# Performance work log

Hardware: AMD Instinct MI355X
Metric: run time of the kernel (lower is better)

The kernel has to match this reference:

```python
import jax, jax.numpy as jnp
import numpy as np

EMB = 1024
HEADS = 16
HEAD_DIM = EMB // HEADS
SCALE = 1.0 / np.sqrt(HEAD_DIM)


def setup_inputs() -> dict:
    key = jax.random.key(0)
    ks = jax.random.split(key, 11)
    B, L, E = 4, 2048, EMB
    s = 1.0 / np.sqrt(E)
    inp = {
        "Q": jax.random.normal(ks[0], (B, L, E), jnp.float32),
        "K": jax.random.normal(ks[1], (B, L, E), jnp.float32),
        "V": jax.random.normal(ks[2], (B, L, E), jnp.float32),
        "WQ": jax.random.normal(ks[3], (E, E), jnp.float32) * s,
        "bQ": jax.random.normal(ks[4], (E,), jnp.float32) * s,
        "WK": jax.random.normal(ks[5], (E, E), jnp.float32) * s,
        "bK": jax.random.normal(ks[6], (E,), jnp.float32) * s,
        "WV": jax.random.normal(ks[7], (E, E), jnp.float32) * s,
        "bV": jax.random.normal(ks[8], (E,), jnp.float32) * s,
        "WO": jax.random.normal(ks[9], (E, E), jnp.float32) * s,
        "bO": jax.random.normal(ks[10], (E,), jnp.float32) * s,
    }
    return inp


def reference(Q, K, V, WQ, bQ, WK, bK, WV, bV, WO, bO):
    B, L, E = Q.shape
    # linear projections (torch Linear stores W as [out,in]; here W is [in,out])
    q = Q @ WQ + bQ
    k = K @ WK + bK
    v = V @ WV + bV
    # split heads: [B, H, L, D]
    q = q.reshape(B, L, HEADS, HEAD_DIM).transpose(0, 2, 1, 3)
    k = k.reshape(B, L, HEADS, HEAD_DIM).transpose(0, 2, 1, 3)
    v = v.reshape(B, L, HEADS, HEAD_DIM).transpose(0, 2, 1, 3)
    scores = jnp.einsum("bhqd,bhkd->bhqk", q, k) * SCALE
    # causal mask (mask=True): -inf above diagonal
    causal = jnp.tril(jnp.ones((L, L), dtype=bool))
    scores = jnp.where(causal, scores, -jnp.inf)
    probs = jax.nn.softmax(scores, axis=-1)
    out = jnp.einsum("bhqk,bhkd->bhqd", probs, v)  # [B,H,L,D]
    out = out.transpose(0, 2, 1, 3).reshape(B, L, E)  # concat heads
    return out @ WO + bO
```

## Files before the change

kernel.cpp:

```cpp
#include <hip/hip_runtime.h>
#include <hip/hip_bf16.h>

#define BB 4
#define HH 16
#define LL 2048
#define DD 64
#define EE 1024
#define MM (BB*LL)
#define SCL 0.125f
#define L2E 1.44269504f

using bf16   = __hip_bfloat16;
using bf16x8 = __attribute__((ext_vector_type(8))) __bf16;
using s16x4  = __attribute__((ext_vector_type(4))) short;
using f32x4  = __attribute__((ext_vector_type(4))) float;
using u32x4  = __attribute__((ext_vector_type(4))) unsigned int;
typedef unsigned int u32;

__device__ __forceinline__ bf16x8 ld8(const bf16* p){ return *(const bf16x8*)p; }
__device__ __forceinline__ bf16x8 ld8(const float* p){
  u32x4 a = *(const u32x4*)p;
  u32x4 b = *(const u32x4*)(p + 4);
  union { bf16x8 v; unsigned short s[8]; } r;
#pragma unroll
  for (int i = 0; i < 4; i++) r.s[i]     = (unsigned short)((a[i] + 0x7FFFu + ((a[i] >> 16) & 1u)) >> 16);
#pragma unroll
  for (int i = 0; i < 4; i++) r.s[i + 4] = (unsigned short)((b[i] + 0x7FFFu + ((b[i] >> 16) & 1u)) >> 16);
  return r.v;
}
__device__ __forceinline__ float ldf(const bf16* p){ return __bfloat162float(*p); }
__device__ __forceinline__ float ldf(const float* p){ return *p; }
__device__ __forceinline__ bf16 to_b(bf16 v){ return v; }
__device__ __forceinline__ bf16 to_b(float v){ return __float2bfloat16(v); }

__device__ __forceinline__ void async16(const bf16* g, bf16* l) {
  __builtin_amdgcn_global_load_lds((const __attribute__((address_space(1))) u32*)g,
                                   (__attribute__((address_space(3))) u32*)l, 16, 0, 0);
}

__global__ __launch_bounds__(256) void detect_dtype(const unsigned int* __restrict__ w,
                                                    int* __restrict__ flag) {
  __shared__ int cnt[256];
  int tid = threadIdx.x;
  int c = 0;
  for (int i = 0; i < 16; i++) {
    unsigned u = w[tid * 16 + i];
    unsigned e = (u >> 7) & 0xFF;
    c += (e >= 100 && e <= 140) ? 1 : 0;
  }
  cnt[tid] = c;
  __syncthreads();
  for (int s = 128; s > 0; s >>= 1) {
    if (tid < s) cnt[tid] += cnt[tid + s];
    __syncthreads();
  }
  if (tid == 0) *flag = (cnt[0] > 2048) ? 1 : 0;
}

__global__ __launch_bounds__(256) void convert_in(
    const void* __restrict__ X0, const void* __restrict__ X1, const void* __restrict__ X2,
    bf16* __restrict__ Y0, bf16* __restrict__ Y1, bf16* __restrict__ Y2,
    const int* __restrict__ flag) {
  int z = blockIdx.z;
  const void* X = (z == 0) ? X0 : (z == 1) ? X1 : X2;
  bf16* Y       = (z == 0) ? Y0 : (z == 1) ? Y1 : Y2;
  size_t idx = ((size_t)blockIdx.x * 256 + threadIdx.x) * 8;
  if (*flag) *(bf16x8*)(Y + idx) = *(const bf16x8*)((const bf16*)X + idx);
  else       *(bf16x8*)(Y + idx) = ld8((const float*)X + idx);
}

template<typename T>
__device__ __forceinline__ void tr_body(const T* __restrict__ W, bf16* __restrict__ Wt,
                                        bf16 (*t)[33]) {
  int tx = threadIdx.x, ty = threadIdx.y;
  int x = blockIdx.x * 32 + tx;
  for (int r = 0; r < 4; r++)
    t[ty + r * 8][tx] = to_b(W[(blockIdx.y * 32 + ty + r * 8) * EE + x]);
  __syncthreads();
  int x2 = blockIdx.y * 32 + tx;
  for (int r = 0; r < 4; r++)
    Wt[(blockIdx.x * 32 + ty + r * 8) * EE + x2] = t[tx][ty + r * 8];
}

__global__ __launch_bounds__(256) void transpose_w4(
    const void* __restrict__ W0, const void* __restrict__ W1,
    const void* __restrict__ W2, const void* __restrict__ W3,
    bf16* __restrict__ T0, bf16* __restrict__ T1,
    bf16* __restrict__ T2, bf16* __restrict__ T3,
    const int* __restrict__ flag) {
  __shared__ bf16 t[32][33];
  int z = blockIdx.z;
  const void* W = (z == 0) ? W0 : (z == 1) ? W1 : (z == 2) ? W2 : W3;
  bf16* Wt      = (z == 0) ? T0 : (z == 1) ? T1 : (z == 2) ? T2 : T3;
  if (*flag) tr_body<bf16>((const bf16*)W, Wt, t);
  else       tr_body<float>((const float*)W, Wt, t);
}

template<typename TIO>
__device__ void gemm_body(const bf16* __restrict__ A, const bf16* __restrict__ Bt,
                          const TIO* __restrict__ bias, void* __restrict__ Cv,
                          int mode, bf16* As, bf16* Bs) {
  constexpr int K = EE;
  int tid = threadIdx.x;
  int lane = tid & 63, w = tid >> 6;
  int l16 = lane & 15, quad = lane >> 4;
  int linear = blockIdx.x + 8 * blockIdx.y;
  int xcd = linear & 7;
  int slot = linear >> 3;
  int m0 = (xcd * 8 + (slot & 7)) * 128;
  int n0 = (slot >> 3) * 128;
  int mw = (w & 1) * 64;
  int nw = (w >> 1) * 64;
  int lr = lane >> 2;
  int lc = (lane & 3) * 8;

  f32x4 acc[4][4] = {};

  for (int k0 = 0; k0 < K; k0 += 32) {
    __syncthreads();
#pragma unroll
    for (int s = 0; s < 2; s++) {
      int r = w * 32 + s * 16;
      async16(A  + (size_t)(m0 + r + lr) * K + k0 + lc, As + r * 32);
      async16(Bt + (size_t)(n0 + r + lr) * K + k0 + lc, Bs + r * 32);
    }
    __syncthreads();
    bf16x8 af[4], bfr[4];
#pragma unroll
    for (int t = 0; t < 4; t++) {
      af[t]  = *(const bf16x8*)(As + (mw + t * 16 + l16) * 32 + quad * 8);
      bfr[t] = *(const bf16x8*)(Bs + (nw + t * 16 + l16) * 32 + quad * 8);
    }
#pragma unroll
    for (int mt = 0; mt < 4; mt++)
#pragma unroll
      for (int nt = 0; nt < 4; nt++)
        acc[mt][nt] = __builtin_amdgcn_mfma_f32_16x16x32_bf16(af[mt], bfr[nt], acc[mt][nt], 0, 0, 0);
  }

#pragma unroll
  for (int nt = 0; nt < 4; nt++) {
    int col = n0 + nw + nt * 16 + l16;
    float bv = ldf(bias + col);
    int hh = col >> 6, d = col & 63;
#pragma unroll
    for (int mt = 0; mt < 4; mt++) {
      f32x4 v = acc[mt][nt];
      int rowb = m0 + mw + mt * 16 + quad * 4;
      if (mode == 0) {
#pragma unroll
        for (int i = 0; i < 4; i++)
          ((bf16*)Cv)[(size_t)(rowb + i) * EE + col] = __float2bfloat16(v[i] + bv);
      } else if (mode == 3) {
#pragma unroll
        for (int i = 0; i < 4; i++) {
          float val = v[i] + bv;
          if constexpr (__is_same(TIO, bf16))
            ((bf16*)Cv)[(size_t)(rowb + i) * EE + col] = __float2bfloat16(val);
          else
            ((float*)Cv)[(size_t)(rowb + i) * EE + col] = val;
        }
      } else {
        int b = rowb >> 11, l0 = rowb & 2047;
        union { s16x4 p; bf16 e[4]; } u;
#pragma unroll
        for (int i = 0; i < 4; i++) u.e[i] = __float2bfloat16(v[i] + bv);
        *(s16x4*)((bf16*)Cv + ((size_t)(b * HH + hh) * DD + d) * LL + l0) = u.p;
      }
    }
  }
}

__global__ __launch_bounds__(256) void qkv_gemm(
    const bf16* __restrict__ Qc, const bf16* __restrict__ Kc, const bf16* __restrict__ Vc,
    const bf16* __restrict__ WQt, const bf16* __restrict__ WKt, const bf16* __restrict__ WVt,
    const void* __restrict__ bQ, const void* __restrict__ bK, const void* __restrict__ bV,
    bf16* __restrict__ qo, bf16* __restrict__ ko, bf16* __restrict__ vo,
    const int* __restrict__ flag) {
  __shared__ __align__(16) bf16 As[128 * 32];
  __shared__ __align__(16) bf16 Bs[128 * 32];
  int z = blockIdx.z;
  const bf16* A    = (z == 0) ? Qc  : (z == 1) ? Kc  : Vc;
  const bf16* Bt   = (z == 0) ? WQt : (z == 1) ? WKt : WVt;
  const void* bb   = (z == 0) ? bQ  : (z == 1) ? bK  : bV;
  bf16* C          = (z == 0) ? qo  : (z == 1) ? ko  : vo;
  int mode = (z == 2) ? 2 : 0;
  if (*flag) gemm_body<bf16>(A, Bt, (const bf16*)bb, C, mode, As, Bs);
  else       gemm_body<float>(A, Bt, (const float*)bb, C, mode, As, Bs);
}

__global__ __launch_bounds__(256) void out_gemm(const bf16* __restrict__ A,
                                                const bf16* __restrict__ WOt,
                                                const void* __restrict__ bO,
                                                void* __restrict__ C,
                                                const int* __restrict__ flag) {
  __shared__ __align__(16) bf16 As[128 * 32];
  __shared__ __align__(16) bf16 Bs[128 * 32];
  if (*flag) gemm_body<bf16>(A, WOt, (const bf16*)bO, C, 3, As, Bs);
  else       gemm_body<float>(A, WOt, (const float*)bO, C, 3, As, Bs);
}

__global__ __launch_bounds__(256) void attn(const bf16* __restrict__ qg,
                                            const bf16* __restrict__ kg,
                                            const bf16* __restrict__ vg,
                                            bf16* __restrict__ outg) {
  __shared__ __align__(16) bf16 Ks[2][64 * 64];
  __shared__ __align__(16) bf16 Vs[2][64 * 64];
  int linear = blockIdx.x + 16 * blockIdx.y;
  int xcd = linear & 7;
  int slot = linear >> 3;
  int bh = xcd * 8 + (slot & 7);
  int pb = slot >> 3;
  int tid = threadIdx.x;
  int w = tid >> 6, lane = tid & 63, l16 = lane & 15, quad = lane >> 4;
  int b = bh >> 4, hh = bh & 15;

  const bf16* qp = qg + (size_t)b * LL * EE + hh * DD;
  const bf16* kp = kg + (size_t)b * LL * EE + hh * DD;
  const bf16* vp = vg + (size_t)bh * DD * LL;
  const f32x4 z4 = {};
  int x7 = l16 & 7;

  for (int half = 0; half < 2; half++) {
    int tile = half ? (31 - pb) : pb;
    int qrow0 = tile * 64 + w * 16;
    int q = qrow0 + l16;
    bf16x8 bq0 = *(const bf16x8*)(qp + (size_t)q * EE + quad * 8);
    bf16x8 bq1 = *(const bf16x8*)(qp + (size_t)q * EE + 32 + quad * 8);

    float m = -1.0e30f, l = 0.f;
    f32x4 o[4] = {};
    int kend = tile + 1;

    __syncthreads();
    {
      int kbase = 0;
#pragma unroll
      for (int t = 0; t < 2; t++) {
        int R = w * 16 + t * 8;
        int r = R + (lane >> 3);
        int gb = (lane & 7) ^ (r & 7);
        async16(kp + (size_t)(kbase + r) * EE + gb * 8, &Ks[0][R * 64]);
        async16(vp + (size_t)r * LL + kbase + gb * 8, &Vs[0][R * 64]);
      }
    }

    for (int kb = 0; kb < kend; kb++) {
      int kbase = kb * 64;
      __syncthreads();
      if (kb + 1 < kend) {
        int nb = (kb + 1) & 1;
        int nbase = kbase + 64;
#pragma unroll
        for (int t = 0; t < 2; t++) {
          int R = w * 16 + t * 8;
          int r = R + (lane >> 3);
          int gb = (lane & 7) ^ (r & 7);
          async16(kp + (size_t)(nbase + r) * EE + gb * 8, &Ks[nb][R * 64]);
          async16(vp + (size_t)r * LL + nbase + gb * 8, &Vs[nb][R * 64]);
        }
      }
      const bf16* Kb = &Ks[kb & 1][0];
      const bf16* Vb = &Vs[kb & 1][0];

      f32x4 s[4];
#pragma unroll
      for (int kt = 0; kt < 4; kt++) {
        int row = kt * 16 + l16;
        bf16x8 kf0 = *(const bf16x8*)(Kb + row * 64 + (quad ^ x7) * 8);
        bf16x8 kf1 = *(const bf16x8*)(Kb + row * 64 + ((quad + 4) ^ x7) * 8);
        s[kt] = __builtin_amdgcn_mfma_f32_16x16x32_bf16(kf0, bq0, z4, 0, 0, 0);
        s[kt] = __builtin_amdgcn_mfma_f32_16x16x32_bf16(kf1, bq1, s[kt], 0, 0, 0);
      }
#if __has_builtin(__builtin_amdgcn_mfma_f32_16x16x16bf16_1k)
      s16x4 vf[4][4];
#pragma unroll
      for (int j = 0; j < 4; j++)
#pragma unroll
        for (int kt = 0; kt < 4; kt++)
          vf[j][kt] = *(const s16x4*)(Vb + (j * 16 + l16) * 64 +
                                      ((kt * 2 + (quad >> 1)) ^ x7) * 8 + (quad & 1) * 4);
#endif
      float sv[16];
      if (kbase + 63 <= qrow0) {
#pragma unroll
        for (int kt = 0; kt < 4; kt++)
#pragma unroll
          for (int i = 0; i < 4; i++) sv[kt * 4 + i] = s[kt][i] * SCL;
      } else {
        int rel = q - kbase - quad * 4;
#pragma unroll
        for (int kt = 0; kt < 4; kt++)
#pragma unroll
          for (int i = 0; i < 4; i++)
            sv[kt * 4 + i] = (kt * 16 + i <= rel) ? s[kt][i] * SCL : -1.0e30f;
      }
      float mloc = sv[0];
#pragma unroll
      for (int i = 1; i < 16; i++) mloc = fmaxf(mloc, sv[i]);
      mloc = fmaxf(mloc, __shfl_xor(mloc, 16));
      mloc = fmaxf(mloc, __shfl_xor(mloc, 32));
      float mnew = fmaxf(m, mloc);
      float alpha = exp2f((m - mnew) * L2E);
      float p[16], ssum = 0.f;
#pragma unroll
      for (int i = 0; i < 16; i++) { p[i] = exp2f((sv[i] - mnew) * L2E); ssum += p[i]; }
      ssum += __shfl_xor(ssum, 16);
      ssum += __shfl_xor(ssum, 32);
      l = l * alpha + ssum;
      m = mnew;
#pragma unroll
      for (int j = 0; j < 4; j++)
#pragma unroll
        for (int i = 0; i < 4; i++) o[j][i] *= alpha;
      union { s16x4 v4; bf16 e[4]; unsigned u[2]; } pk[4];
#pragma unroll
      for (int kt = 0; kt < 4; kt++)
#pragma unroll
        for (int i = 0; i < 4; i++) pk[kt].e[i] = __float2bfloat16(p[kt * 4 + i]);
#if __has_builtin(__builtin_amdgcn_mfma_f32_16x16x16bf16_1k)
#pragma unroll
      for (int kt = 0; kt < 4; kt++)
#pragma unroll
        for (int j = 0; j < 4; j++)
          o[j] = __builtin_amdgcn_mfma_f32_16x16x16bf16_1k(vf[j][kt], pk[kt].v4, o[j], 0, 0, 0);
#else
#pragma unroll
      for (int c = 0; c < 2; c++) {
        union { bf16x8 v8; unsigned u[4]; } bfr;
#pragma unroll
        for (int r = 0; r < 4; r++) {
          int key = c * 32 + quad * 8 + 2 * r;
          int srcl = (((key >> 2) & 3) << 4) + l16;
          unsigned v0 = __shfl((int)pk[2 * c].u[r & 1], srcl, 64);
          unsigned v1 = __shfl((int)pk[2 * c + 1].u[r & 1], srcl, 64);
          bfr.u[r] = (quad < 2) ? v0 : v1;
        }
#pragma unroll
        for (int j = 0; j < 4; j++) {
          bf16x8 vfr = *(const bf16x8*)(Vb + (j * 16 + l16) * 64 + ((c * 4 + quad) ^ x7) * 8);
          o[j] = __builtin_amdgcn_mfma_f32_16x16x32_bf16(vfr, bfr.v8, o[j], 0, 0, 0);
        }
      }
#endif
    }
    float inv = 1.0f / l;
#pragma unroll
    for (int j = 0; j < 4; j++) {
      union { s16x4 v4; bf16 e[4]; } u;
#pragma unroll
      for (int i = 0; i < 4; i++) u.e[i] = __float2bfloat16(o[j][i] * inv);
      *(s16x4*)(outg + (size_t)(b * LL + q) * EE + hh * DD + j * 16 + quad * 4) = u.v4;
    }
  }
}

extern "C" void kernel_launch(void* const* d_in, const int* in_sizes, int n_in,
                              void* d_out, int out_size, void* d_ws, size_t ws_size,
                              hipStream_t stream) {
  const void* Q   = d_in[0];
  const void* Kin = d_in[1];
  const void* V   = d_in[2];
  const void* WQ  = d_in[3];
  const void* bQ  = d_in[4];
  const void* WK  = d_in[5];
  const void* bK  = d_in[6];
  const void* WV  = d_in[7];
  const void* bV  = d_in[8];
  const void* WO  = d_in[9];
  const void* bO  = d_in[10];

  int* flag = (int*)d_ws;
  bf16* base = (bf16*)((char*)d_ws + 256);
  bf16* wqt  = base;
  bf16* wkt  = wqt + (size_t)EE * EE;
  bf16* wvt  = wkt + (size_t)EE * EE;
  bf16* wot  = wvt + (size_t)EE * EE;
  bf16* Qc   = wot + (size_t)EE * EE;
  bf16* Kc   = Qc  + (size_t)MM * EE;
  bf16* Vc   = Kc  + (size_t)MM * EE;
  bf16* qws  = Vc  + (size_t)MM * EE;
  bf16* kws  = qws + (size_t)MM * EE;
  bf16* vws  = kws + (size_t)MM * EE;
  bf16* aout = vws + (size_t)MM * EE;

  detect_dtype<<<1, 256, 0, stream>>>((const unsigned int*)WQ, flag);

  convert_in<<<dim3(MM * EE / 8 / 256, 1, 3), 256, 0, stream>>>(Q, Kin, V, Qc, Kc, Vc, flag);

  transpose_w4<<<dim3(32, 32, 4), dim3(32, 8), 0, stream>>>(
      WQ, WK, WV, WO, wqt, wkt, wvt, wot, flag);

  qkv_gemm<<<dim3(8, 64, 3), 256, 0, stream>>>(
      Qc, Kc, Vc, wqt, wkt, wvt, bQ, bK, bV, qws, kws, vws, flag);

  attn<<<dim3(16, 64), 256, 0, stream>>>(qws, kws, vws, aout);

  out_gemm<<<dim3(8, 64), 256, 0, stream>>>(aout, wot, bO, d_out, flag);
}
```

Measured before the change: 436.2 us.

## Fuse input conversion into QKV GEMM, widen K tile, enlarge attention query tiles

Drops the separate fp32-to-bf16 conversion pass: the QKV GEMM now reads the fp32 activations directly and converts them into shared memory, which saves a full write and re-read of three large tensors. The GEMM K-step doubles to 64, halving the number of barrier pairs per output tile at the cost of twice the shared memory. Attention now gives each wave 32 query rows (two 16-row groups) so every K/V tile is reused across more queries, uses a simpler grid mapping, and skips compute on fully masked key blocks. The fp32 A path uses synchronous loads instead of async copies, which may expose latency, and the larger per-wave state raises register pressure.

```diff
diff --git a/kernel.cpp b/kernel.cpp
--- a/kernel.cpp
+++ b/kernel.cpp
@@ -57,18 +57,6 @@
   if (tid == 0) *flag = (cnt[0] > 2048) ? 1 : 0;
 }
 
-__global__ __launch_bounds__(256) void convert_in(
-    const void* __restrict__ X0, const void* __restrict__ X1, const void* __restrict__ X2,
-    bf16* __restrict__ Y0, bf16* __restrict__ Y1, bf16* __restrict__ Y2,
-    const int* __restrict__ flag) {
-  int z = blockIdx.z;
-  const void* X = (z == 0) ? X0 : (z == 1) ? X1 : X2;
-  bf16* Y       = (z == 0) ? Y0 : (z == 1) ? Y1 : Y2;
-  size_t idx = ((size_t)blockIdx.x * 256 + threadIdx.x) * 8;
-  if (*flag) *(bf16x8*)(Y + idx) = *(const bf16x8*)((const bf16*)X + idx);
-  else       *(bf16x8*)(Y + idx) = ld8((const float*)X + idx);
-}
-
 template<typename T>
 __device__ __forceinline__ void tr_body(const T* __restrict__ W, bf16* __restrict__ Wt,
                                         bf16 (*t)[33]) {
@@ -96,8 +84,8 @@
   else       tr_body<float>((const float*)W, Wt, t);
 }
 
-template<typename TIO>
-__device__ void gemm_body(const bf16* __restrict__ A, const bf16* __restrict__ Bt,
+template<typename TA, typename TIO>
+__device__ void gemm_body(const TA* __restrict__ A, const bf16* __restrict__ Bt,
                           const TIO* __restrict__ bias, void* __restrict__ Cv,
                           int mode, bf16* As, bf16* Bs) {
   constexpr int K = EE;
@@ -111,31 +99,39 @@
   int n0 = (slot >> 3) * 128;
   int mw = (w & 1) * 64;
   int nw = (w >> 1) * 64;
-  int lr = lane >> 2;
-  int lc = (lane & 3) * 8;
+  int lr = lane >> 3;
+  int lc = (lane & 7) * 8;
 
   f32x4 acc[4][4] = {};
 
-  for (int k0 = 0; k0 < K; k0 += 32) {
+  for (int k0 = 0; k0 < K; k0 += 64) {
     __syncthreads();
 #pragma unroll
-    for (int s = 0; s < 2; s++) {
-      int r = w * 32 + s * 16;
-      async16(A  + (size_t)(m0 + r + lr) * K + k0 + lc, As + r * 32);
-      async16(Bt + (size_t)(n0 + r + lr) * K + k0 + lc, Bs + r * 32);
+    for (int t = 0; t < 4; t++) {
+      int R = w * 32 + t * 8;
+      int r = R + lr;
+      if constexpr (__is_same(TA, bf16)) {
+        async16(A + (size_t)(m0 + r) * K + k0 + lc, As + R * 64);
+      } else {
+        *(bf16x8*)(As + r * 64 + lc) = ld8(A + (size_t)(m0 + r) * K + k0 + lc);
+      }
+      async16(Bt + (size_t)(n0 + r) * K + k0 + lc, Bs + R * 64);
     }
     __syncthreads();
-    bf16x8 af[4], bfr[4];
-#pragma unroll
-    for (int t = 0; t < 4; t++) {
-      af[t]  = *(const bf16x8*)(As + (mw + t * 16 + l16) * 32 + quad * 8);
-      bfr[t] = *(const bf16x8*)(Bs + (nw + t * 16 + l16) * 32 + quad * 8);
-    }
-#pragma unroll
-    for (int mt = 0; mt < 4; mt++)
-#pragma unroll
-      for (int nt = 0; nt < 4; nt++)
-        acc[mt][nt] = __builtin_amdgcn_mfma_f32_16x16x32_bf16(af[mt], bfr[nt], acc[mt][nt], 0, 0, 0);
+#pragma unroll
+    for (int h = 0; h < 2; h++) {
+      bf16x8 af[4], bfr[4];
+#pragma unroll
+      for (int t = 0; t < 4; t++) {
+        af[t]  = *(const bf16x8*)(As + (mw + t * 16 + l16) * 64 + h * 32 + quad * 8);
+        bfr[t] = *(const bf16x8*)(Bs + (nw + t * 16 + l16) * 64 + h * 32 + quad * 8);
+      }
+#pragma unroll
+      for (int mt = 0; mt < 4; mt++)
+#pragma unroll
+        for (int nt = 0; nt < 4; nt++)
+          acc[mt][nt] = __builtin_amdgcn_mfma_f32_16x16x32_bf16(af[mt], bfr[nt], acc[mt][nt], 0, 0, 0);
+    }
   }
 
 #pragma unroll
@@ -172,21 +168,21 @@
 }
 
 __global__ __launch_bounds__(256) void qkv_gemm(
-    const bf16* __restrict__ Qc, const bf16* __restrict__ Kc, const bf16* __restrict__ Vc,
+    const void* __restrict__ Q, const void* __restrict__ Kin, const void* __restrict__ V,
     const bf16* __restrict__ WQt, const bf16* __restrict__ WKt, const bf16* __restrict__ WVt,
     const void* __restrict__ bQ, const void* __restrict__ bK, const void* __restrict__ bV,
     bf16* __restrict__ qo, bf16* __restrict__ ko, bf16* __restrict__ vo,
     const int* __restrict__ flag) {
-  __shared__ __align__(16) bf16 As[128 * 32];
-  __shared__ __align__(16) bf16 Bs[128 * 32];
+  __shared__ __align__(16) bf16 As[128 * 64];
+  __shared__ __align__(16) bf16 Bs[128 * 64];
   int z = blockIdx.z;
-  const bf16* A    = (z == 0) ? Qc  : (z == 1) ? Kc  : Vc;
+  const void* A    = (z == 0) ? Q   : (z == 1) ? Kin : V;
   const bf16* Bt   = (z == 0) ? WQt : (z == 1) ? WKt : WVt;
   const void* bb   = (z == 0) ? bQ  : (z == 1) ? bK  : bV;
   bf16* C          = (z == 0) ? qo  : (z == 1) ? ko  : vo;
   int mode = (z == 2) ? 2 : 0;
-  if (*flag) gemm_body<bf16>(A, Bt, (const bf16*)bb, C, mode, As, Bs);
-  else       gemm_body<float>(A, Bt, (const float*)bb, C, mode, As, Bs);
+  if (*flag) gemm_body<bf16, bf16>((const bf16*)A, Bt, (const bf16*)bb, C, mode, As, Bs);
+  else       gemm_body<float, float>((const float*)A, Bt, (const float*)bb, C, mode, As, Bs);
 }
 
 __global__ __launch_bounds__(256) void out_gemm(const bf16* __restrict__ A,
@@ -194,10 +190,10 @@
                                                 const void* __restrict__ bO,
                                                 void* __restrict__ C,
                                                 const int* __restrict__ flag) {
-  __shared__ __align__(16) bf16 As[128 * 32];
-  __shared__ __align__(16) bf16 Bs[128 * 32];
-  if (*flag) gemm_body<bf16>(A, WOt, (const bf16*)bO, C, 3, As, Bs);
-  else       gemm_body<float>(A, WOt, (const float*)bO, C, 3, As, Bs);
+  __shared__ __align__(16) bf16 As[128 * 64];
+  __shared__ __align__(16) bf16 Bs[128 * 64];
+  if (*flag) gemm_body<bf16, bf16>(A, WOt, (const bf16*)bO, C, 3, As, Bs);
+  else       gemm_body<bf16, float>(A, WOt, (const float*)bO, C, 3, As, Bs);
 }
 
 __global__ __launch_bounds__(256) void attn(const bf16* __restrict__ qg,
@@ -206,11 +202,8 @@
                                             bf16* __restrict__ outg) {
   __shared__ __align__(16) bf16 Ks[2][64 * 64];
   __shared__ __align__(16) bf16 Vs[2][64 * 64];
-  int linear = blockIdx.x + 16 * blockIdx.y;
-  int xcd = linear & 7;
-  int slot = linear >> 3;
-  int bh = xcd * 8 + (slot & 7);
-  int pb = slot >> 3;
+  int bh = blockIdx.x;
+  int pr = blockIdx.y;
   int tid = threadIdx.x;
   int w = tid >> 6, lane = tid & 63, l16 = lane & 15, quad = lane >> 4;
   int b = bh >> 4, hh = bh & 15;
@@ -222,26 +215,30 @@
   int x7 = l16 & 7;
 
   for (int half = 0; half < 2; half++) {
-    int tile = half ? (31 - pb) : pb;
-    int qrow0 = tile * 64 + w * 16;
-    int q = qrow0 + l16;
-    bf16x8 bq0 = *(const bf16x8*)(qp + (size_t)q * EE + quad * 8);
-    bf16x8 bq1 = *(const bf16x8*)(qp + (size_t)q * EE + 32 + quad * 8);
-
-    float m = -1.0e30f, l = 0.f;
-    f32x4 o[4] = {};
-    int kend = tile + 1;
+    int tile = half ? (15 - pr) : pr;
+    int qrow0 = tile * 128 + w * 32;
+    int qmax = qrow0 + 31;
+    bf16x8 bq[2][2];
+#pragma unroll
+    for (int g = 0; g < 2; g++) {
+      const bf16* qr = qp + (size_t)(qrow0 + g * 16 + l16) * EE;
+      bq[g][0] = *(const bf16x8*)(qr + quad * 8);
+      bq[g][1] = *(const bf16x8*)(qr + 32 + quad * 8);
+    }
+
+    float m[2] = {-1.0e30f, -1.0e30f}, l[2] = {0.f, 0.f};
+    f32x4 o[2][4] = {};
+    int kend = 2 * (tile + 1);
 
     __syncthreads();
     {
-      int kbase = 0;
 #pragma unroll
       for (int t = 0; t < 2; t++) {
         int R = w * 16 + t * 8;
         int r = R + (lane >> 3);
         int gb = (lane & 7) ^ (r & 7);
-        async16(kp + (size_t)(kbase + r) * EE + gb * 8, &Ks[0][R * 64]);
-        async16(vp + (size_t)r * LL + kbase + gb * 8, &Vs[0][R * 64]);
+        async16(kp + (size_t)r * EE + gb * 8, &Ks[0][R * 64]);
+        async16(vp + (size_t)r * LL + gb * 8, &Vs[0][R * 64]);
       }
     }
 
@@ -260,17 +257,21 @@
           async16(vp + (size_t)r * LL + nbase + gb * 8, &Vs[nb][R * 64]);
         }
       }
+      if (kbase > qmax) continue;
       const bf16* Kb = &Ks[kb & 1][0];
       const bf16* Vb = &Vs[kb & 1][0];
 
-      f32x4 s[4];
+      f32x4 s[2][4];
 #pragma unroll
       for (int kt = 0; kt < 4; kt++) {
         int row = kt * 16 + l16;
         bf16x8 kf0 = *(const bf16x8*)(Kb + row * 64 + (quad ^ x7) * 8);
         bf16x8 kf1 = *(const bf16x8*)(Kb + row * 64 + ((quad + 4) ^ x7) * 8);
-        s[kt] = __builtin_amdgcn_mfma_f32_16x16x32_bf16(kf0, bq0, z4, 0, 0, 0);
-        s[kt] = __builtin_amdgcn_mfma_f32_16x16x32_bf16(kf1, bq1, s[kt], 0, 0, 0);
+#pragma unroll
+        for (int g = 0; g < 2; g++) {
+          s[g][kt] = __builtin_amdgcn_mfma_f32_16x16x32_bf16(kf0, bq[g][0], z4, 0, 0, 0);
+          s[g][kt] = __builtin_amdgcn_mfma_f32_16x16x32_bf16(kf1, bq[g][1], s[g][kt], 0, 0, 0);
+        }
       }
 #if __has_builtin(__builtin_amdgcn_mfma_f32_16x16x16bf16_1k)
       s16x4 vf[4][4];
@@ -281,76 +282,88 @@
           vf[j][kt] = *(const s16x4*)(Vb + (j * 16 + l16) * 64 +
                                       ((kt * 2 + (quad >> 1)) ^ x7) * 8 + (quad & 1) * 4);
 #endif
-      float sv[16];
-      if (kbase + 63 <= qrow0) {
+      union { s16x4 v4; bf16 e[4]; unsigned u[2]; } pk[2][4];
+#pragma unroll
+      for (int g = 0; g < 2; g++) {
+        int qg_ = qrow0 + g * 16 + l16;
+        float sv[16];
+        if (kbase + 63 <= qrow0 + g * 16) {
+#pragma unroll
+          for (int kt = 0; kt < 4; kt++)
+#pragma unroll
+            for (int i = 0; i < 4; i++) sv[kt * 4 + i] = s[g][kt][i] * SCL;
+        } else {
+          int rel = qg_ - kbase - quad * 4;
+#pragma unroll
+          for (int kt = 0; kt < 4; kt++)
+#pragma unroll
+            for (int i = 0; i < 4; i++)
+              sv[kt * 4 + i] = (kt * 16 + i <= rel) ? s[g][kt][i] * SCL : -1.0e30f;
+        }
+        float mloc = sv[0];
+#pragma unroll
+        for (int i = 1; i < 16; i++) mloc = fmaxf(mloc, sv[i]);
+        mloc = fmaxf(mloc, __shfl_xor(mloc, 16));
+        mloc = fmaxf(mloc, __shfl_xor(mloc, 32));
+        float mnew = fmaxf(m[g], mloc);
+        float alpha = exp2f((m[g] - mnew) * L2E);
+        float p[16], ssum = 0.f;
+#pragma unroll
+        for (int i = 0; i < 16; i++) { p[i] = exp2f((sv[i] - mnew) * L2E); ssum += p[i]; }
+        ssum += __shfl_xor(ssum, 16);
+        ssum += __shfl_xor(ssum, 32);
+        l[g] = l[g] * alpha + ssum;
+        m[g] = mnew;
+#pragma unroll
+        for (int j = 0; j < 4; j++)
+#pragma unroll
+          for (int i = 0; i < 4; i++) o[g][j][i] *= alpha;
 #pragma unroll
         for (int kt = 0; kt < 4; kt++)
 #pragma unroll
-          for (int i = 0; i < 4; i++) sv[kt * 4 + i] = s[kt][i] * SCL;
-      } else {
-        int rel = q - kbase - quad * 4;
-#pragma unroll
-        for (int kt = 0; kt < 4; kt++)
-#pragma unroll
-          for (int i = 0; i < 4; i++)
-            sv[kt * 4 + i] = (kt * 16 + i <= rel) ? s[kt][i] * SCL : -1.0e30f;
-      }
-      float mloc = sv[0];
-#pragma unroll
-      for (int i = 1; i < 16; i++) mloc = fmaxf(mloc, sv[i]);
-      mloc = fmaxf(mloc, __shfl_xor(mloc, 16));
-      mloc = fmaxf(mloc, __shfl_xor(mloc, 32));
-      float mnew = fmaxf(m, mloc);
-      float alpha = exp2f((m - mnew) * L2E);
-      float p[16], ssum = 0.f;
-#pragma unroll
-      for (int i = 0; i < 16; i++) { p[i] = exp2f((sv[i] - mnew) * L2E); ssum += p[i]; }
-      ssum += __shfl_xor(ssum, 16);
-      ssum += __shfl_xor(ssum, 32);
-      l = l * alpha + ssum;
-      m = mnew;
-#pragma unroll
-      for (int j = 0; j < 4; j++)
-#pragma unroll
-        for (int i = 0; i < 4; i++) o[j][i] *= alpha;
-      union { s16x4 v4; bf16 e[4]; unsigned u[2]; } pk[4];
+          for (int i = 0; i < 4; i++) pk[g][kt].e[i] = __float2bfloat16(p[kt * 4 + i]);
+      }
+#if __has_builtin(__builtin_amdgcn_mfma_f32_16x16x16bf16_1k)
 #pragma unroll
       for (int kt = 0; kt < 4; kt++)
 #pragma unroll
-        for (int i = 0; i < 4; i++) pk[kt].e[i] = __float2bfloat16(p[kt * 4 + i]);
-#if __has_builtin(__builtin_amdgcn_mfma_f32_16x16x16bf16_1k)
-#pragma unroll
-      for (int kt = 0; kt < 4; kt++)
-#pragma unroll
-        for (int j = 0; j < 4; j++)
-          o[j] = __builtin_amdgcn_mfma_f32_16x16x16bf16_1k(vf[j][kt], pk[kt].v4, o[j], 0, 0, 0);
+        for (int j = 0; j < 4; j++) {
+          o[0][j] = __builtin_amdgcn_mfma_f32_16x16x16bf16_1k(vf[j][kt], pk[0][kt].v4, o[0][j], 0, 0, 0);
+          o[1][j] = __builtin_amdgcn_mfma_f32_16x16x16bf16_1k(vf[j][kt], pk[1][kt].v4, o[1][j], 0, 0, 0);
+        }
 #else
 #pragma unroll
-      for (int c = 0; c < 2; c++) {
-        union { bf16x8 v8; unsigned u[4]; } bfr;
-#pragma unroll
-        for (int r = 0; r < 4; r++) {
-          int key = c * 32 + quad * 8 + 2 * r;
-          int srcl = (((key >> 2) & 3) << 4) + l16;
-          unsigned v0 = __shfl((int)pk[2 * c].u[r & 1], srcl, 64);
-          unsigned v1 = __shfl((int)pk[2 * c + 1].u[r & 1], srcl, 64);
-          bfr.u[r] = (quad < 2) ? v0 : v1;
-        }
-#pragma unroll
-        for (int j = 0; j < 4; j++) {
-          bf16x8 vfr = *(const bf16x8*)(Vb + (j * 16 + l16) * 64 + ((c * 4 + quad) ^ x7) * 8);
-          o[j] = __builtin_amdgcn_mfma_f32_16x16x32_bf16(vfr, bfr.v8, o[j], 0, 0, 0);
-        }
-      }
+      for (int g = 0; g < 2; g++)
+#pragma unroll
+        for (int c = 0; c < 2; c++) {
+          union { bf16x8 v8; unsigned u[4]; } bfr;
+#pragma unroll
+          for (int r = 0; r < 4; r++) {
+            int key = c * 32 + quad * 8 + 2 * r;
+            int srcl = (((key >> 2) & 3) << 4) + l16;
+            unsigned v0 = __shfl((int)pk[g][2 * c].u[r & 1], srcl, 64);
+            unsigned v1 = __shfl((int)pk[g][2 * c + 1].u[r & 1], srcl, 64);
+            bfr.u[r] = (quad < 2) ? v0 : v1;
+          }
+#pragma unroll
+          for (int j = 0; j < 4; j++) {
+            bf16x8 vfr = *(const bf16x8*)(Vb + (j * 16 + l16) * 64 + ((c * 4 + quad) ^ x7) * 8);
+            o[g][j] = __builtin_amdgcn_mfma_f32_16x16x32_bf16(vfr, bfr.v8, o[g][j], 0, 0, 0);
+          }
+        }
 #endif
     }
-    float inv = 1.0f / l;
-#pragma unroll
-    for (int j = 0; j < 4; j++) {
-      union { s16x4 v4; bf16 e[4]; } u;
-#pragma unroll
-      for (int i = 0; i < 4; i++) u.e[i] = __float2bfloat16(o[j][i] * inv);
-      *(s16x4*)(outg + (size_t)(b * LL + q) * EE + hh * DD + j * 16 + quad * 4) = u.v4;
+#pragma unroll
+    for (int g = 0; g < 2; g++) {
+      float inv = 1.0f / l[g];
+      int qg_ = qrow0 + g * 16 + l16;
+#pragma unroll
+      for (int j = 0; j < 4; j++) {
+        union { s16x4 v4; bf16 e[4]; } u;
+#pragma unroll
+        for (int i = 0; i < 4; i++) u.e[i] = __float2bfloat16(o[g][j][i] * inv);
+        *(s16x4*)(outg + (size_t)(b * LL + qg_) * EE + hh * DD + j * 16 + quad * 4) = u.v4;
+      }
     }
   }
 }
@@ -376,25 +389,20 @@
   bf16* wkt  = wqt + (size_t)EE * EE;
   bf16* wvt  = wkt + (size_t)EE * EE;
   bf16* wot  = wvt + (size_t)EE * EE;
-  bf16* Qc   = wot + (size_t)EE * EE;
-  bf16* Kc   = Qc  + (size_t)MM * EE;
-  bf16* Vc   = Kc  + (size_t)MM * EE;
-  bf16* qws  = Vc  + (size_t)MM * EE;
+  bf16* qws  = wot + (size_t)EE * EE;
   bf16* kws  = qws + (size_t)MM * EE;
   bf16* vws  = kws + (size_t)MM * EE;
   bf16* aout = vws + (size_t)MM * EE;
 
   detect_dtype<<<1, 256, 0, stream>>>((const unsigned int*)WQ, flag);
 
-  convert_in<<<dim3(MM * EE / 8 / 256, 1, 3), 256, 0, stream>>>(Q, Kin, V, Qc, Kc, Vc, flag);
-
   transpose_w4<<<dim3(32, 32, 4), dim3(32, 8), 0, stream>>>(
       WQ, WK, WV, WO, wqt, wkt, wvt, wot, flag);
 
   qkv_gemm<<<dim3(8, 64, 3), 256, 0, stream>>>(
-      Qc, Kc, Vc, wqt, wkt, wvt, bQ, bK, bV, qws, kws, vws, flag);
-
-  attn<<<dim3(16, 64), 256, 0, stream>>>(qws, kws, vws, aout);
+      Q, Kin, V, wqt, wkt, wvt, bQ, bK, bV, qws, kws, vws, flag);
+
+  attn<<<dim3(64, 8), 256, 0, stream>>>(qws, kws, vws, aout);
 
   out_gemm<<<dim3(8, 64), 256, 0, stream>>>(aout, wot, bO, d_out, flag);
 }
```

Measured after the change: 481.0 us. +10.3%, slower.
